# Kernel tuning notes

Hardware: AMD Instinct MI355X
Metric: run time of the kernel (lower is better)

## Reference

```python
import jax, jax.numpy as jnp
import numpy as np


def _2div(arr):
    arr_res = arr.copy()
    arr_pieces = []
    pa = 0
    st = 0
    needdivcnt = 0
    for i, a in enumerate(arr):
        if a != pa:
            arr_pieces.append([st, i])
            if i - st != 1:
                needdivcnt += 1
            pa = a
            st = i
    arr_pieces.append([st, len(arr)])
    if len(arr) - st != 1:
        needdivcnt += 1
    offset = range(len(arr_pieces), len(arr_pieces) + needdivcnt)
    p = 0
    for arr_p in arr_pieces:
        length = arr_p[1] - arr_p[0]
        if length == 1:
            continue
        half_len = int(np.ceil(length / 2))
        for j in range(arr_p[0] + half_len, arr_p[1]):
            arr_res[j] = offset[p]
        p += 1
    return arr_res


def get_division_tree(n_agents):
    agent2divitreeindex = np.arange(n_agents)
    np.random.shuffle(agent2divitreeindex)
    max_div = np.ceil(np.log2(n_agents)).astype(int)
    levels = np.zeros(shape=(max_div + 1, n_agents), dtype=int)
    for ith in range(1, len(levels)):
        levels[ith, :] = _2div(levels[ith - 1, :])
    res_levels = levels.copy()
    for i, idx in enumerate(agent2divitreeindex):
        res_levels[:, i] = levels[:, idx]
    return res_levels


def setup_inputs() -> dict:
    B, A, H, NACT = 2048, 50, 512, 64
    F = H + A  # in-features of first Linear (hidden + one-hot agent id)
    np.random.seed(0)
    div_tree = get_division_tree(A)
    routing = jnp.asarray(div_tree[-1], dtype=jnp.int32)  # max_level routing: agent -> net index
    key = jax.random.key(0)
    k0, k1, k2 = jax.random.split(key, 3)
    x_in = jax.random.normal(k0, (B, A, H), dtype=jnp.float32)
    # stacked per-net parameters (n_nets == n_agent independent 2-layer MLPs)
    W1 = jax.random.normal(k1, (A, F, H), dtype=jnp.float32) * (1.0 / np.sqrt(F))
    b1 = jnp.zeros((A, H), dtype=jnp.float32)
    W2 = jax.random.normal(k2, (A, H, NACT), dtype=jnp.float32) * (1.0 / np.sqrt(H))
    b2 = jnp.zeros((A, NACT), dtype=jnp.float32)
    return {"x_in": x_in, "W1": W1, "b1": b1, "W2": W2, "b2": b2, "routing": routing}


def reference(x_in, W1, b1, W2, b2, routing):
    # x_in: [B, A, H]; routing: [A] int (which net each agent uses)
    B, A, H = x_in.shape
    # add_onehot_id_at_last_dim: append agent-id one-hot -> [B, A, H+A]
    onehot = jnp.broadcast_to(jnp.eye(A, dtype=x_in.dtype), (B, A, A))
    x0 = jnp.concatenate([x_in, onehot], axis=-1)
    # gather routed expert weights per agent
    W1r, b1r = W1[routing], b1[routing]   # [A, H+A, H], [A, H]
    W2r, b2r = W2[routing], b2[routing]   # [A, H, NACT], [A, NACT]
    h = jax.nn.relu(jnp.einsum('baf,afh->bah', x0, W1r) + b1r)
    out = jnp.einsum('bah,ahn->ban', h, W2r) + b2r  # [B, A, NACT]
    return out
```

## Files before the change

kernel.cpp:

```cpp
#include <hip/hip_runtime.h>

typedef __attribute__((ext_vector_type(8))) short bf16x8;
typedef __attribute__((ext_vector_type(4))) float f32x4;
typedef __attribute__((ext_vector_type(4))) unsigned short u16x4;
typedef __attribute__((ext_vector_type(8))) unsigned short u16x8;

#define B_ 2048
#define A_ 50
#define H_ 512
#define NACT_ 64
#define F_ 562
#define BM_ 64
#define BK_ 32
#define NSTEP_ (H_ / BK_)

#define WS_W1T 0
#define WS_W2T ((size_t)A_ * H_ * H_ * 2)
#define WS_B1 (WS_W2T + (size_t)A_ * NACT_ * H_ * 2)
#define WS_B2 (WS_B1 + (size_t)A_ * H_ * 4)

static __device__ __forceinline__ unsigned short f2bf(float f) {
  unsigned int u = __builtin_bit_cast(unsigned int, f);
  u += 0x7fffu + ((u >> 16) & 1u);
  return (unsigned short)(u >> 16);
}

static __device__ __forceinline__ void gld_lds16(const unsigned short* src,
                                                 unsigned short* dst) {
  __builtin_amdgcn_global_load_lds(
      (const __attribute__((address_space(1))) unsigned int*)(const void*)src,
      (__attribute__((address_space(3))) unsigned int*)(void*)dst, 16, 0, 0);
}

static __device__ __forceinline__ int clamp_r(int r) {
  return r < 0 ? 0 : (r > A_ - 1 ? A_ - 1 : r);
}

__global__ void prep_w1(const float* __restrict__ w1,
                        const int* __restrict__ routing,
                        unsigned short* __restrict__ w1t) {
  const int bid = blockIdx.x;
  const int a = bid / 64;
  const int tile = bid - a * 64;
  const int tk = tile & 7, tj = tile >> 3;
  const int k0 = tk * 64, j0 = tj * 64;
  const int r = clamp_r(routing[a]);
  __shared__ float tl[64][65];
  const int t = threadIdx.x;
  const int c = t & 63, q = t >> 6;
#pragma unroll
  for (int i = 0; i < 16; ++i) {
    const int kl = q + i * 4;
    tl[kl][c] = w1[((size_t)r * F_ + k0 + kl) * H_ + j0 + c];
  }
  __syncthreads();
#pragma unroll
  for (int it = 0; it < 2; ++it) {
    const int jl = t >> 2, c2 = t & 3;
    const int kc = it * 4 + (c2 ^ (jl & 3));
    u16x8 v;
#pragma unroll
    for (int e = 0; e < 8; ++e) v[e] = f2bf(tl[kc * 8 + e][jl]);
    unsigned short* dst = w1t +
        (((size_t)a * 16 + tk * 2 + it) * H_ + j0 + jl) * 32 + c2 * 8;
    *(u16x8*)dst = v;
  }
}

__global__ void prep_w2(const float* __restrict__ w2,
                        const int* __restrict__ routing,
                        unsigned short* __restrict__ w2t) {
  const int bid = blockIdx.x;
  const int a = bid >> 3;
  const int tk = bid & 7;
  const int k0 = tk * 64;
  const int r = clamp_r(routing[a]);
  __shared__ float tl[64][65];
  const int t = threadIdx.x;
  const int c = t & 63, q = t >> 6;
#pragma unroll
  for (int i = 0; i < 16; ++i) {
    const int kl = q + i * 4;
    tl[kl][c] = w2[((size_t)r * H_ + k0 + kl) * NACT_ + c];
  }
  __syncthreads();
#pragma unroll
  for (int i = 0; i < 16; ++i) {
    const int nl = q + i * 4;
    w2t[((size_t)a * NACT_ + nl) * H_ + k0 + c] = f2bf(tl[c][nl]);
  }
}

__global__ void prep_bias(const float* __restrict__ w1,
                          const float* __restrict__ b1,
                          const float* __restrict__ b2,
                          const int* __restrict__ routing,
                          float* __restrict__ bias1, float* __restrict__ bias2) {
  const int a = blockIdx.x;
  const int t = threadIdx.x;
  const int r = clamp_r(routing[a]);
  bias1[a * H_ + t] = b1[(size_t)r * H_ + t] + w1[((size_t)r * F_ + H_ + a) * H_ + t];
  if (t < NACT_) bias2[a * NACT_ + t] = b2[r * NACT_ + t];
}

__global__ __launch_bounds__(512, 4) void divtree_main(
    const float* __restrict__ x, const unsigned short* __restrict__ w1t,
    const unsigned short* __restrict__ w2t, const float* __restrict__ bias1,
    const float* __restrict__ bias2, float* __restrict__ out) {
  __shared__ union {
    struct {
      unsigned short w1[2][H_ * BK_];
      unsigned short xs[2][BM_ * BK_];
    } st;
    unsigned short h[BM_ * H_];
    float outb[BM_][66];
  } sm;

  const int bid = blockIdx.x;
  const int swz = (bid & 7) * 200 + (bid >> 3);
  const int a = swz >> 5;
  const int mblk = swz & 31;
  const int b0 = mblk * BM_;

  const int tid = threadIdx.x;
  const int lane = tid & 63;
  const int w = tid >> 6;
  const int l16 = lane & 15;
  const int lk = lane >> 4;
  const int sxor = lk ^ (l16 & 3);

  const int wj = w * 64;

  const unsigned short* w1ta = w1t + (size_t)a * (H_ * H_);

  const int xrow = tid >> 3;
  const int xq = tid & 7;
  const float* xbase =
      x + ((size_t)(b0 + xrow) * A_ + (size_t)a) * H_ + (size_t)xq * 4;
  const int xs_off = xrow * BK_ + ((xq >> 1) ^ (xrow & 3)) * 8 + (xq & 1) * 4;

  const int afr_base = (wj + l16) * BK_ + sxor * 8;
  const int bfr_base = l16 * BK_ + sxor * 8;

  f32x4 acc[4][4];
#pragma unroll
  for (int i = 0; i < 4; ++i)
#pragma unroll
    for (int j = 0; j < 4; ++j) acc[i][j] = (f32x4){0.f, 0.f, 0.f, 0.f};

  f32x4 xr[3];

  {
    const f32x4 xv0 = *(const f32x4*)xbase;
#pragma unroll
    for (int i = 0; i < 4; ++i)
      gld_lds16(w1ta + ((size_t)(i * 512 + tid) << 3),
                sm.st.w1[0] + (size_t)(i * 512 + (w << 6)) * 8);
    xr[1] = *(const f32x4*)(xbase + 1 * BK_);
    xr[2] = *(const f32x4*)(xbase + 2 * BK_);
    u16x4 v;
#pragma unroll
    for (int e = 0; e < 4; ++e) v[e] = f2bf(xv0[e]);
    *(u16x4*)(sm.st.xs[0] + xs_off) = v;
  }

#pragma unroll
  for (int t = 0; t < NSTEP_; ++t) {
    const int buf = t & 1;
    if (t <= NSTEP_ - 3)
      asm volatile("s_waitcnt vmcnt(1) lgkmcnt(0)" ::: "memory");
    else
      asm volatile("s_waitcnt vmcnt(0) lgkmcnt(0)" ::: "memory");
    __builtin_amdgcn_sched_barrier(0);
    __builtin_amdgcn_s_barrier();
    __builtin_amdgcn_sched_barrier(0);
    if (t + 1 < NSTEP_) {
      const unsigned short* wsrc = w1ta + (size_t)(t + 1) * (H_ * BK_);
      unsigned short* wdst = sm.st.w1[buf ^ 1];
#pragma unroll
      for (int i = 0; i < 4; ++i)
        gld_lds16(wsrc + ((size_t)(i * 512 + tid) << 3),
                  wdst + (size_t)(i * 512 + (w << 6)) * 8);
    }
    if (t + 3 < NSTEP_)
      xr[(t + 3) % 3] = *(const f32x4*)(xbase + (size_t)(t + 3) * BK_);
    const unsigned short* w1s = sm.st.w1[buf];
    const unsigned short* xss = sm.st.xs[buf];
    bf16x8 bfr[4];
#pragma unroll
    for (int mf = 0; mf < 4; ++mf)
      bfr[mf] = *(const bf16x8*)(xss + bfr_base + mf * (16 * BK_));
    __builtin_amdgcn_s_setprio(1);
#pragma unroll
    for (int jf = 0; jf < 4; ++jf) {
      const bf16x8 afr = *(const bf16x8*)(w1s + afr_base + jf * (16 * BK_));
#pragma unroll
      for (int mf = 0; mf < 4; ++mf)
        acc[jf][mf] = __builtin_amdgcn_mfma_f32_16x16x32_bf16(
            afr, bfr[mf], acc[jf][mf], 0, 0, 0);
    }
    __builtin_amdgcn_s_setprio(0);
    if (t + 1 < NSTEP_) {
      const f32x4 xv = xr[(t + 1) % 3];
      u16x4 v;
#pragma unroll
      for (int e = 0; e < 4; ++e) v[e] = f2bf(xv[e]);
      *(u16x4*)(sm.st.xs[buf ^ 1] + xs_off) = v;
    }
  }
  __syncthreads();

  const float* b1p = bias1 + a * H_;
#pragma unroll
  for (int jf = 0; jf < 4; ++jf) {
    const f32x4 bv = *(const f32x4*)(b1p + wj + jf * 16 + lk * 4);
    const int cbase = (wj >> 3) + jf * 2 + (lk >> 1);
    const int half4 = (lk & 1) * 4;
#pragma unroll
    for (int mf = 0; mf < 4; ++mf) {
      u16x4 hv;
#pragma unroll
      for (int r = 0; r < 4; ++r) {
        float f = acc[jf][mf][r] + bv[r];
        f = f > 0.f ? f : 0.f;
        hv[r] = f2bf(f);
      }
      const int m = mf * 16 + l16;
      const int off = m * H_ + ((cbase ^ (l16 & 7))) * 8 + half4;
      *(u16x4*)(sm.h + off) = hv;
    }
  }
  __syncthreads();

  const int m0 = (w & 1) * 32;
  const int n0 = (w >> 1) * 16;
  const unsigned short* w2p =
      w2t + ((size_t)a * NACT_ + n0 + l16) * H_ + lk * 8;
  f32x4 acc2[2];
  acc2[0] = (f32x4){0.f, 0.f, 0.f, 0.f};
  acc2[1] = (f32x4){0.f, 0.f, 0.f, 0.f};
#pragma unroll
  for (int kf = 0; kf < 16; ++kf) {
    const bf16x8 bf2 = *(const bf16x8*)(w2p + kf * 32);
#pragma unroll
    for (int mf = 0; mf < 2; ++mf) {
      const int row = m0 + mf * 16 + l16;
      const int off = row * H_ + (((kf * 4 + lk) ^ (l16 & 7))) * 8;
      const bf16x8 af2 = *(const bf16x8*)(sm.h + off);
      acc2[mf] = __builtin_amdgcn_mfma_f32_16x16x32_bf16(af2, bf2, acc2[mf],
                                                         0, 0, 0);
    }
  }
  const float b2v = bias2[a * NACT_ + n0 + l16];
  __syncthreads();
#pragma unroll
  for (int mf = 0; mf < 2; ++mf)
#pragma unroll
    for (int r = 0; r < 4; ++r)
      sm.outb[m0 + mf * 16 + lk * 4 + r][n0 + l16] = acc2[mf][r] + b2v;
  __syncthreads();

  {
    const int row = tid >> 3;
    const int q8 = (tid & 7) * 8;
    const f32x4 v0 = *(const f32x4*)(&sm.outb[row][q8]);
    const f32x4 v1 = *(const f32x4*)(&sm.outb[row][q8 + 4]);
    float* op = out + ((size_t)(b0 + row) * A_ + a) * NACT_ + q8;
    *(f32x4*)op = v0;
    *(f32x4*)(op + 4) = v1;
  }
}

extern "C" void kernel_launch(void* const* d_in, const int* in_sizes, int n_in,
                              void* d_out, int out_size, void* d_ws,
                              size_t ws_size, hipStream_t stream) {
  const float* x = (const float*)d_in[0];
  const float* w1 = (const float*)d_in[1];
  const float* b1 = (const float*)d_in[2];
  const float* w2 = (const float*)d_in[3];
  const float* b2 = (const float*)d_in[4];
  const int* routing = (const int*)d_in[5];
  float* out = (float*)d_out;

  char* ws = (char*)d_ws;
  unsigned short* w1t = (unsigned short*)(ws + WS_W1T);
  unsigned short* w2t = (unsigned short*)(ws + WS_W2T);
  float* bias1 = (float*)(ws + WS_B1);
  float* bias2 = (float*)(ws + WS_B2);

  prep_w1<<<A_ * 64, 256, 0, stream>>>(w1, routing, w1t);
  prep_w2<<<A_ * 8, 256, 0, stream>>>(w2, routing, w2t);
  prep_bias<<<A_, 512, 0, stream>>>(w1, b1, b2, routing, bias1, bias2);
  divtree_main<<<A_ * (B_ / BM_), 512, 0, stream>>>(x, w1t, w2t, bias1, bias2,
                                                    out);
}
```

Baseline: 143.2 us.

## Double tile to BM=128, BK=64 with single-buffered x and split-K barriers

Doubles the batch rows per block to 128 and the K-step to 64, so each block reuses every streamed W1 tile across twice as many rows and does half as many pipeline steps. The W1 workspace layout and its XOR swizzle change to match the 64-wide K chunk. The x tile goes from double-buffered to single-buffered, with a mid-step barrier placed so the next x tile can be written after the second half-K of reads, and the second-layer GEMM is retiled across 8 waves. Accumulator registers per thread double and occupancy drops to 2 blocks per CU (launch bound 4 to 2), and there are half as many blocks, which may hurt latency hiding and leave the GPU less evenly loaded.

```diff
diff --git a/kernel.cpp b/kernel.cpp
--- a/kernel.cpp
+++ b/kernel.cpp
@@ -10,8 +10,8 @@
 #define H_ 512
 #define NACT_ 64
 #define F_ 562
-#define BM_ 64
-#define BK_ 32
+#define BM_ 128
+#define BK_ 64
 #define NSTEP_ (H_ / BK_)
 
 #define WS_W1T 0
@@ -57,12 +57,13 @@
 #pragma unroll
   for (int it = 0; it < 2; ++it) {
     const int jl = t >> 2, c2 = t & 3;
-    const int kc = it * 4 + (c2 ^ (jl & 3));
+    const int p = it * 4 + c2;
+    const int cl = p ^ (jl & 7);
     u16x8 v;
 #pragma unroll
-    for (int e = 0; e < 8; ++e) v[e] = f2bf(tl[kc * 8 + e][jl]);
-    unsigned short* dst = w1t +
-        (((size_t)a * 16 + tk * 2 + it) * H_ + j0 + jl) * 32 + c2 * 8;
+    for (int e = 0; e < 8; ++e) v[e] = f2bf(tl[cl * 8 + e][jl]);
+    unsigned short* dst =
+        w1t + (((size_t)a * 8 + tk) * H_ + j0 + jl) * 64 + p * 8;
     *(u16x8*)dst = v;
   }
 }
@@ -103,23 +104,23 @@
   if (t < NACT_) bias2[a * NACT_ + t] = b2[r * NACT_ + t];
 }
 
-__global__ __launch_bounds__(512, 4) void divtree_main(
+__global__ __launch_bounds__(512, 2) void divtree_main(
     const float* __restrict__ x, const unsigned short* __restrict__ w1t,
     const unsigned short* __restrict__ w2t, const float* __restrict__ bias1,
     const float* __restrict__ bias2, float* __restrict__ out) {
   __shared__ union {
     struct {
       unsigned short w1[2][H_ * BK_];
-      unsigned short xs[2][BM_ * BK_];
+      unsigned short xs[BM_ * BK_];
     } st;
     unsigned short h[BM_ * H_];
     float outb[BM_][66];
   } sm;
 
   const int bid = blockIdx.x;
-  const int swz = (bid & 7) * 200 + (bid >> 3);
-  const int a = swz >> 5;
-  const int mblk = swz & 31;
+  const int swz = (bid & 7) * 100 + (bid >> 3);
+  const int a = swz >> 4;
+  const int mblk = swz & 15;
   const int b0 = mblk * BM_;
 
   const int tid = threadIdx.x;
@@ -127,94 +128,140 @@
   const int w = tid >> 6;
   const int l16 = lane & 15;
   const int lk = lane >> 4;
-  const int sxor = lk ^ (l16 & 3);
-
-  const int wj = w * 64;
+  const int l7 = l16 & 7;
+
+  const int wnq = w & 3;
+  const int wm = w >> 2;
 
   const unsigned short* w1ta = w1t + (size_t)a * (H_ * H_);
 
-  const int xrow = tid >> 3;
-  const int xq = tid & 7;
+  const int xrow = tid >> 2;
+  const int xseg = tid & 3;
   const float* xbase =
-      x + ((size_t)(b0 + xrow) * A_ + (size_t)a) * H_ + (size_t)xq * 4;
-  const int xs_off = xrow * BK_ + ((xq >> 1) ^ (xrow & 3)) * 8 + (xq & 1) * 4;
-
-  const int afr_base = (wj + l16) * BK_ + sxor * 8;
-  const int bfr_base = l16 * BK_ + sxor * 8;
-
-  f32x4 acc[4][4];
-#pragma unroll
-  for (int i = 0; i < 4; ++i)
+      x + ((size_t)(b0 + xrow) * A_ + (size_t)a) * H_ + (size_t)xseg * 16;
+  const int xp0 = (xseg * 2) ^ (xrow & 7);
+  const int xp1 = (xseg * 2 + 1) ^ (xrow & 7);
+  unsigned short* xs0 = sm.st.xs + xrow * BK_;
+
+  f32x4 acc[8][4];
+#pragma unroll
+  for (int i = 0; i < 8; ++i)
 #pragma unroll
     for (int j = 0; j < 4; ++j) acc[i][j] = (f32x4){0.f, 0.f, 0.f, 0.f};
 
-  f32x4 xr[3];
+  f32x4 xr[2][4];
 
   {
-    const f32x4 xv0 = *(const f32x4*)xbase;
-#pragma unroll
-    for (int i = 0; i < 4; ++i)
+    f32x4 x0[4];
+#pragma unroll
+    for (int i = 0; i < 4; ++i) x0[i] = *(const f32x4*)(xbase + i * 4);
+#pragma unroll
+    for (int i = 0; i < 8; ++i)
       gld_lds16(w1ta + ((size_t)(i * 512 + tid) << 3),
                 sm.st.w1[0] + (size_t)(i * 512 + (w << 6)) * 8);
-    xr[1] = *(const f32x4*)(xbase + 1 * BK_);
-    xr[2] = *(const f32x4*)(xbase + 2 * BK_);
-    u16x4 v;
-#pragma unroll
-    for (int e = 0; e < 4; ++e) v[e] = f2bf(xv0[e]);
-    *(u16x4*)(sm.st.xs[0] + xs_off) = v;
+    u16x8 v0, v1;
+#pragma unroll
+    for (int e = 0; e < 4; ++e) {
+      v0[e] = f2bf(x0[0][e]); v0[4 + e] = f2bf(x0[1][e]);
+      v1[e] = f2bf(x0[2][e]); v1[4 + e] = f2bf(x0[3][e]);
+    }
+    *(u16x8*)(xs0 + xp0 * 8) = v0;
+    *(u16x8*)(xs0 + xp1 * 8) = v1;
+#pragma unroll
+    for (int i = 0; i < 4; ++i)
+      xr[1][i] = *(const f32x4*)(xbase + 1 * BK_ + i * 4);
+    asm volatile("s_waitcnt vmcnt(4) lgkmcnt(0)" ::: "memory");
+    __builtin_amdgcn_sched_barrier(0);
+    __builtin_amdgcn_s_barrier();
+    __builtin_amdgcn_sched_barrier(0);
   }
 
 #pragma unroll
   for (int t = 0; t < NSTEP_; ++t) {
     const int buf = t & 1;
-    if (t <= NSTEP_ - 3)
-      asm volatile("s_waitcnt vmcnt(1) lgkmcnt(0)" ::: "memory");
+    if (t + 1 < NSTEP_) {
+      const unsigned short* wsrc = w1ta + (size_t)(t + 1) * (H_ * BK_);
+      unsigned short* wdst = sm.st.w1[buf ^ 1];
+#pragma unroll
+      for (int i = 0; i < 8; ++i)
+        gld_lds16(wsrc + ((size_t)(i * 512 + tid) << 3),
+                  wdst + (size_t)(i * 512 + (w << 6)) * 8);
+    }
+    const unsigned short* w1s = sm.st.w1[buf];
+    {
+      bf16x8 afr[8], bfr[4];
+#pragma unroll
+      for (int jf = 0; jf < 8; ++jf)
+        afr[jf] = *(const bf16x8*)(w1s + (wnq * 128 + jf * 16 + l16) * 64 +
+                                   ((0 * 4 + lk) ^ l7) * 8);
+#pragma unroll
+      for (int mf = 0; mf < 4; ++mf)
+        bfr[mf] = *(const bf16x8*)(sm.st.xs + (wm * 64 + mf * 16 + l16) * 64 +
+                                   ((0 * 4 + lk) ^ l7) * 8);
+      __builtin_amdgcn_s_setprio(1);
+#pragma unroll
+      for (int jf = 0; jf < 8; ++jf)
+#pragma unroll
+        for (int mf = 0; mf < 4; ++mf)
+          acc[jf][mf] = __builtin_amdgcn_mfma_f32_16x16x32_bf16(
+              afr[jf], bfr[mf], acc[jf][mf], 0, 0, 0);
+      __builtin_amdgcn_s_setprio(0);
+    }
+    {
+      bf16x8 afr[8], bfr[4];
+#pragma unroll
+      for (int jf = 0; jf < 8; ++jf)
+        afr[jf] = *(const bf16x8*)(w1s + (wnq * 128 + jf * 16 + l16) * 64 +
+                                   ((1 * 4 + lk) ^ l7) * 8);
+#pragma unroll
+      for (int mf = 0; mf < 4; ++mf)
+        bfr[mf] = *(const bf16x8*)(sm.st.xs + (wm * 64 + mf * 16 + l16) * 64 +
+                                   ((1 * 4 + lk) ^ l7) * 8);
+      asm volatile("s_waitcnt lgkmcnt(0)" ::: "memory");
+      __builtin_amdgcn_sched_barrier(0);
+      __builtin_amdgcn_s_barrier();
+      __builtin_amdgcn_s_setprio(1);
+#pragma unroll
+      for (int jf = 0; jf < 8; ++jf)
+#pragma unroll
+        for (int mf = 0; mf < 4; ++mf)
+          acc[jf][mf] = __builtin_amdgcn_mfma_f32_16x16x32_bf16(
+              afr[jf], bfr[mf], acc[jf][mf], 0, 0, 0);
+      __builtin_amdgcn_s_setprio(0);
+    }
+    if (t + 1 < NSTEP_) {
+      asm volatile("s_waitcnt vmcnt(8)" ::: "memory");
+      __builtin_amdgcn_sched_barrier(0);
+      u16x8 v0, v1;
+#pragma unroll
+      for (int e = 0; e < 4; ++e) {
+        v0[e] = f2bf(xr[(t + 1) & 1][0][e]);
+        v0[4 + e] = f2bf(xr[(t + 1) & 1][1][e]);
+        v1[e] = f2bf(xr[(t + 1) & 1][2][e]);
+        v1[4 + e] = f2bf(xr[(t + 1) & 1][3][e]);
+      }
+      *(u16x8*)(xs0 + xp0 * 8) = v0;
+      *(u16x8*)(xs0 + xp1 * 8) = v1;
+    }
+    if (t + 2 < NSTEP_) {
+#pragma unroll
+      for (int i = 0; i < 4; ++i)
+        xr[t & 1][i] = *(const f32x4*)(xbase + (size_t)(t + 2) * BK_ + i * 4);
+    }
+    if (t + 2 < NSTEP_)
+      asm volatile("s_waitcnt vmcnt(4) lgkmcnt(0)" ::: "memory");
     else
       asm volatile("s_waitcnt vmcnt(0) lgkmcnt(0)" ::: "memory");
     __builtin_amdgcn_sched_barrier(0);
     __builtin_amdgcn_s_barrier();
     __builtin_amdgcn_sched_barrier(0);
-    if (t + 1 < NSTEP_) {
-      const unsigned short* wsrc = w1ta + (size_t)(t + 1) * (H_ * BK_);
-      unsigned short* wdst = sm.st.w1[buf ^ 1];
-#pragma unroll
-      for (int i = 0; i < 4; ++i)
-        gld_lds16(wsrc + ((size_t)(i * 512 + tid) << 3),
-                  wdst + (size_t)(i * 512 + (w << 6)) * 8);
-    }
-    if (t + 3 < NSTEP_)
-      xr[(t + 3) % 3] = *(const f32x4*)(xbase + (size_t)(t + 3) * BK_);
-    const unsigned short* w1s = sm.st.w1[buf];
-    const unsigned short* xss = sm.st.xs[buf];
-    bf16x8 bfr[4];
-#pragma unroll
-    for (int mf = 0; mf < 4; ++mf)
-      bfr[mf] = *(const bf16x8*)(xss + bfr_base + mf * (16 * BK_));
-    __builtin_amdgcn_s_setprio(1);
-#pragma unroll
-    for (int jf = 0; jf < 4; ++jf) {
-      const bf16x8 afr = *(const bf16x8*)(w1s + afr_base + jf * (16 * BK_));
-#pragma unroll
-      for (int mf = 0; mf < 4; ++mf)
-        acc[jf][mf] = __builtin_amdgcn_mfma_f32_16x16x32_bf16(
-            afr, bfr[mf], acc[jf][mf], 0, 0, 0);
-    }
-    __builtin_amdgcn_s_setprio(0);
-    if (t + 1 < NSTEP_) {
-      const f32x4 xv = xr[(t + 1) % 3];
-      u16x4 v;
-#pragma unroll
-      for (int e = 0; e < 4; ++e) v[e] = f2bf(xv[e]);
-      *(u16x4*)(sm.st.xs[buf ^ 1] + xs_off) = v;
-    }
-  }
-  __syncthreads();
+  }
 
   const float* b1p = bias1 + a * H_;
 #pragma unroll
-  for (int jf = 0; jf < 4; ++jf) {
-    const f32x4 bv = *(const f32x4*)(b1p + wj + jf * 16 + lk * 4);
-    const int cbase = (wj >> 3) + jf * 2 + (lk >> 1);
+  for (int jf = 0; jf < 8; ++jf) {
+    const f32x4 bv = *(const f32x4*)(b1p + wnq * 128 + jf * 16 + lk * 4);
+    const int cJ = wnq * 16 + jf * 2 + (lk >> 1);
     const int half4 = (lk & 1) * 4;
 #pragma unroll
     for (int mf = 0; mf < 4; ++mf) {
@@ -225,49 +272,63 @@
         f = f > 0.f ? f : 0.f;
         hv[r] = f2bf(f);
       }
-      const int m = mf * 16 + l16;
-      const int off = m * H_ + ((cbase ^ (l16 & 7))) * 8 + half4;
+      const int m = wm * 64 + mf * 16 + l16;
+      const int off = m * H_ + ((cJ ^ (m & 7))) * 8 + half4;
       *(u16x4*)(sm.h + off) = hv;
     }
   }
   __syncthreads();
 
-  const int m0 = (w & 1) * 32;
-  const int n0 = (w >> 1) * 16;
-  const unsigned short* w2p =
-      w2t + ((size_t)a * NACT_ + n0 + l16) * H_ + lk * 8;
-  f32x4 acc2[2];
-  acc2[0] = (f32x4){0.f, 0.f, 0.f, 0.f};
-  acc2[1] = (f32x4){0.f, 0.f, 0.f, 0.f};
+  const int m0 = (w >> 1) * 32;
+  const int n0 = (w & 1) * 32;
+  f32x4 acc2[2][2];
+#pragma unroll
+  for (int i = 0; i < 2; ++i)
+#pragma unroll
+    for (int j = 0; j < 2; ++j) acc2[i][j] = (f32x4){0.f, 0.f, 0.f, 0.f};
 #pragma unroll
   for (int kf = 0; kf < 16; ++kf) {
-    const bf16x8 bf2 = *(const bf16x8*)(w2p + kf * 32);
+    bf16x8 bf2[2], af2[2];
+#pragma unroll
+    for (int nf = 0; nf < 2; ++nf)
+      bf2[nf] = *(const bf16x8*)(w2t +
+                                 ((size_t)a * NACT_ + n0 + nf * 16 + l16) * H_ +
+                                 kf * 32 + lk * 8);
 #pragma unroll
     for (int mf = 0; mf < 2; ++mf) {
       const int row = m0 + mf * 16 + l16;
-      const int off = row * H_ + (((kf * 4 + lk) ^ (l16 & 7))) * 8;
-      const bf16x8 af2 = *(const bf16x8*)(sm.h + off);
-      acc2[mf] = __builtin_amdgcn_mfma_f32_16x16x32_bf16(af2, bf2, acc2[mf],
-                                                         0, 0, 0);
-    }
-  }
-  const float b2v = bias2[a * NACT_ + n0 + l16];
+      af2[mf] = *(const bf16x8*)(sm.h + row * H_ +
+                                 (((kf * 4 + lk) ^ (l16 & 7))) * 8);
+    }
+#pragma unroll
+    for (int mf = 0; mf < 2; ++mf)
+#pragma unroll
+      for (int nf = 0; nf < 2; ++nf)
+        acc2[mf][nf] = __builtin_amdgcn_mfma_f32_16x16x32_bf16(
+            af2[mf], bf2[nf], acc2[mf][nf], 0, 0, 0);
+  }
+  float b2v[2];
+#pragma unroll
+  for (int nf = 0; nf < 2; ++nf)
+    b2v[nf] = bias2[a * NACT_ + n0 + nf * 16 + l16];
   __syncthreads();
 #pragma unroll
   for (int mf = 0; mf < 2; ++mf)
 #pragma unroll
-    for (int r = 0; r < 4; ++r)
-      sm.outb[m0 + mf * 16 + lk * 4 + r][n0 + l16] = acc2[mf][r] + b2v;
+    for (int nf = 0; nf < 2; ++nf)
+#pragma unroll
+      for (int r = 0; r < 4; ++r)
+        sm.outb[m0 + mf * 16 + lk * 4 + r][n0 + nf * 16 + l16] =
+            acc2[mf][nf][r] + b2v[nf];
   __syncthreads();
 
   {
-    const int row = tid >> 3;
-    const int q8 = (tid & 7) * 8;
-    const f32x4 v0 = *(const f32x4*)(&sm.outb[row][q8]);
-    const f32x4 v1 = *(const f32x4*)(&sm.outb[row][q8 + 4]);
-    float* op = out + ((size_t)(b0 + row) * A_ + a) * NACT_ + q8;
-    *(f32x4*)op = v0;
-    *(f32x4*)(op + 4) = v1;
+    const int row = tid >> 2;
+    const int sg = (tid & 3) * 16;
+    float* op = out + ((size_t)(b0 + row) * A_ + a) * NACT_ + sg;
+#pragma unroll
+    for (int i = 0; i < 4; ++i)
+      *(f32x4*)(op + i * 4) = *(const f32x4*)(&sm.outb[row][sg + i * 4]);
   }
 }
 
```

After: 174.8 us. +22.1%, slower.

## Split fused MLP into two tiled GEMM kernels with a bf16 hidden buffer

Applied to the files above, without the earlier changes.

Replaces the single fused kernel, which handled 64 batch rows against the full 512-wide hidden layer, with two kernels. The first computes layer 1 in 128x128 tiles and writes bf16 hidden activations to workspace. The second reads them back for layer 2 in 128-row tiles with a reswizzled W2 layout. The intent is more reuse per tile and better occupancy. The cost is an extra round trip of about 100MB of hidden activations through global memory, and the new path only runs when the workspace is large enough, otherwise it falls back to the old kernel.

```diff
diff --git a/kernel.cpp b/kernel.cpp
--- a/kernel.cpp
+++ b/kernel.cpp
@@ -10,14 +10,13 @@
 #define H_ 512
 #define NACT_ 64
 #define F_ 562
-#define BM_ 64
-#define BK_ 32
-#define NSTEP_ (H_ / BK_)
 
 #define WS_W1T 0
 #define WS_W2T ((size_t)A_ * H_ * H_ * 2)
 #define WS_B1 (WS_W2T + (size_t)A_ * NACT_ * H_ * 2)
 #define WS_B2 (WS_B1 + (size_t)A_ * H_ * 4)
+#define WS_H (WS_B2 + (size_t)A_ * NACT_ * 4)
+#define WS_NEED (WS_H + (size_t)B_ * A_ * H_ * 2)
 
 static __device__ __forceinline__ unsigned short f2bf(float f) {
   unsigned int u = __builtin_bit_cast(unsigned int, f);
@@ -36,9 +35,9 @@
   return r < 0 ? 0 : (r > A_ - 1 ? A_ - 1 : r);
 }
 
-__global__ void prep_w1(const float* __restrict__ w1,
-                        const int* __restrict__ routing,
-                        unsigned short* __restrict__ w1t) {
+__global__ void prep_w1_n(const float* __restrict__ w1,
+                          const int* __restrict__ routing,
+                          unsigned short* __restrict__ w1t) {
   const int bid = blockIdx.x;
   const int a = bid / 64;
   const int tile = bid - a * 64;
@@ -54,22 +53,23 @@
     tl[kl][c] = w1[((size_t)r * F_ + k0 + kl) * H_ + j0 + c];
   }
   __syncthreads();
+  const int jl = t >> 2, pq = t & 3;
+  const int sx = (jl >> 1) & 3;
 #pragma unroll
   for (int it = 0; it < 2; ++it) {
-    const int jl = t >> 2, c2 = t & 3;
-    const int kc = it * 4 + (c2 ^ (jl & 3));
+    const int cc = pq ^ sx;
     u16x8 v;
 #pragma unroll
-    for (int e = 0; e < 8; ++e) v[e] = f2bf(tl[kc * 8 + e][jl]);
-    unsigned short* dst = w1t +
-        (((size_t)a * 16 + tk * 2 + it) * H_ + j0 + jl) * 32 + c2 * 8;
+    for (int e = 0; e < 8; ++e) v[e] = f2bf(tl[it * 32 + cc * 8 + e][jl]);
+    unsigned short* dst =
+        w1t + (((size_t)a * 16 + tk * 2 + it) * H_ + j0 + jl) * 32 + pq * 8;
     *(u16x8*)dst = v;
   }
 }
 
-__global__ void prep_w2(const float* __restrict__ w2,
-                        const int* __restrict__ routing,
-                        unsigned short* __restrict__ w2t) {
+__global__ void prep_w2_n(const float* __restrict__ w2,
+                          const int* __restrict__ routing,
+                          unsigned short* __restrict__ w2t) {
   const int bid = blockIdx.x;
   const int a = bid >> 3;
   const int tk = bid & 7;
@@ -84,10 +84,17 @@
     tl[kl][c] = w2[((size_t)r * H_ + k0 + kl) * NACT_ + c];
   }
   __syncthreads();
-#pragma unroll
-  for (int i = 0; i < 16; ++i) {
-    const int nl = q + i * 4;
-    w2t[((size_t)a * NACT_ + nl) * H_ + k0 + c] = f2bf(tl[c][nl]);
+  const int n = t >> 2, pq0 = t & 3;
+#pragma unroll
+  for (int it = 0; it < 2; ++it) {
+    const int p = it * 4 + pq0;
+    const int cc = p ^ (n & 7);
+    u16x8 v;
+#pragma unroll
+    for (int e = 0; e < 8; ++e) v[e] = f2bf(tl[cc * 8 + e][n]);
+    unsigned short* dst =
+        w2t + (((size_t)a * 8 + tk) * NACT_ + n) * 64 + p * 8;
+    *(u16x8*)dst = v;
   }
 }
 
@@ -103,104 +110,410 @@
   if (t < NACT_) bias2[a * NACT_ + t] = b2[r * NACT_ + t];
 }
 
-__global__ __launch_bounds__(512, 4) void divtree_main(
+__global__ __launch_bounds__(256, 3) void k1_l1(
+    const float* __restrict__ x, const unsigned short* __restrict__ w1t,
+    const float* __restrict__ bias1, unsigned short* __restrict__ h_ws) {
+  __shared__ union {
+    struct {
+      unsigned short w1s[2][128 * 32];
+      unsigned short xs[2][128 * 32];
+    } st;
+    unsigned short hl[128 * 128];
+  } sm;
+
+  const int bid = blockIdx.x;
+  const int swz = (bid & 7) * 400 + (bid >> 3);
+  const int a = swz >> 6;
+  const int rem = swz & 63;
+  const int mt = rem >> 2, jt = rem & 3;
+  const int b0 = mt * 128, j0g = jt * 128;
+
+  const int tid = threadIdx.x;
+  const int lane = tid & 63;
+  const int w = tid >> 6;
+  const int l16 = lane & 15;
+  const int lk = lane >> 4;
+  const int sxor = lk ^ ((l16 >> 1) & 3);
+
+  const int wj = (w & 1) * 64, wm = (w >> 1) * 64;
+
+  const unsigned short* w1src =
+      w1t + (size_t)a * (16 * H_ * 32) + (size_t)j0g * 32;
+
+  const int xrow = tid >> 1, xhalf = tid & 1;
+  const float* xp =
+      x + ((size_t)(b0 + xrow) * A_ + (size_t)a) * H_ + xhalf * 16;
+  const int xsrow = xrow * 32;
+  const int xpos0 = (xhalf * 2) ^ ((xrow >> 1) & 3);
+
+  const int afr_off = (wj + l16) * 32 + sxor * 8;
+  const int bfr_off = (wm + l16) * 32 + sxor * 8;
+
+  f32x4 acc[4][4];
+#pragma unroll
+  for (int i = 0; i < 4; ++i)
+#pragma unroll
+    for (int j = 0; j < 4; ++j) acc[i][j] = (f32x4){0.f, 0.f, 0.f, 0.f};
+
+  {
+    f32x4 xv[4];
+#pragma unroll
+    for (int i = 0; i < 4; ++i) xv[i] = *(const f32x4*)(xp + i * 4);
+#pragma unroll
+    for (int i = 0; i < 2; ++i) {
+      const int idx = i * 256 + tid;
+      gld_lds16(w1src + (size_t)(idx >> 2) * 32 + (idx & 3) * 8,
+                sm.st.w1s[0] + idx * 8);
+    }
+    u16x8 v0, v1;
+#pragma unroll
+    for (int e = 0; e < 4; ++e) {
+      v0[e] = f2bf(xv[0][e]); v0[4 + e] = f2bf(xv[1][e]);
+      v1[e] = f2bf(xv[2][e]); v1[4 + e] = f2bf(xv[3][e]);
+    }
+    *(u16x8*)(sm.st.xs[0] + xsrow + xpos0 * 8) = v0;
+    *(u16x8*)(sm.st.xs[0] + xsrow + (xpos0 ^ 1) * 8) = v1;
+  }
+  __syncthreads();
+
+#pragma unroll 2
+  for (int t = 0; t < 16; ++t) {
+    const int buf = t & 1;
+    f32x4 xv[4];
+    if (t < 15) {
+      const float* p = xp + (t + 1) * 32;
+#pragma unroll
+      for (int i = 0; i < 4; ++i) xv[i] = *(const f32x4*)(p + i * 4);
+      const unsigned short* wsrc = w1src + (size_t)(t + 1) * (H_ * 32);
+#pragma unroll
+      for (int i = 0; i < 2; ++i) {
+        const int idx = i * 256 + tid;
+        gld_lds16(wsrc + (size_t)(idx >> 2) * 32 + (idx & 3) * 8,
+                  sm.st.w1s[buf ^ 1] + idx * 8);
+      }
+    }
+    {
+      const unsigned short* w1s = sm.st.w1s[buf];
+      const unsigned short* xss = sm.st.xs[buf];
+      bf16x8 afr[4], bfr[4];
+#pragma unroll
+      for (int jf = 0; jf < 4; ++jf)
+        afr[jf] = *(const bf16x8*)(w1s + afr_off + jf * (16 * 32));
+#pragma unroll
+      for (int mf = 0; mf < 4; ++mf)
+        bfr[mf] = *(const bf16x8*)(xss + bfr_off + mf * (16 * 32));
+#pragma unroll
+      for (int jf = 0; jf < 4; ++jf)
+#pragma unroll
+        for (int mf = 0; mf < 4; ++mf)
+          acc[jf][mf] = __builtin_amdgcn_mfma_f32_16x16x32_bf16(
+              afr[jf], bfr[mf], acc[jf][mf], 0, 0, 0);
+    }
+    if (t < 15) {
+      u16x8 v0, v1;
+#pragma unroll
+      for (int e = 0; e < 4; ++e) {
+        v0[e] = f2bf(xv[0][e]); v0[4 + e] = f2bf(xv[1][e]);
+        v1[e] = f2bf(xv[2][e]); v1[4 + e] = f2bf(xv[3][e]);
+      }
+      *(u16x8*)(sm.st.xs[buf ^ 1] + xsrow + xpos0 * 8) = v0;
+      *(u16x8*)(sm.st.xs[buf ^ 1] + xsrow + (xpos0 ^ 1) * 8) = v1;
+    }
+    __syncthreads();
+  }
+
+  const float* b1p = bias1 + a * H_ + j0g;
+#pragma unroll
+  for (int jf = 0; jf < 4; ++jf) {
+    const f32x4 bv = *(const f32x4*)(b1p + wj + jf * 16 + lk * 4);
+    const int cJ = (wj >> 3) + jf * 2 + (lk >> 1);
+    const int half4 = (lk & 1) * 4;
+#pragma unroll
+    for (int mf = 0; mf < 4; ++mf) {
+      u16x4 hv;
+#pragma unroll
+      for (int r = 0; r < 4; ++r) {
+        float f = acc[jf][mf][r] + bv[r];
+        f = f > 0.f ? f : 0.f;
+        hv[r] = f2bf(f);
+      }
+      const int m = wm + mf * 16 + l16;
+      const int p = (cJ & 8) | ((cJ & 7) ^ (m & 7));
+      *(u16x4*)(sm.hl + m * 128 + p * 8 + half4) = hv;
+    }
+  }
+  __syncthreads();
+  {
+    const int m = tid >> 1, half = tid & 1;
+    unsigned short* rowbase =
+        h_ws + ((size_t)a * B_ + b0 + m) * H_ + (jt * 2 + half) * 64;
+    const unsigned short* lsrc = sm.hl + m * 128 + half * 64;
+#pragma unroll
+    for (int p = 0; p < 8; ++p)
+      *(u16x8*)(rowbase + p * 8) = *(const u16x8*)(lsrc + p * 8);
+  }
+}
+
+__global__ __launch_bounds__(256, 3) void k2_l2(
+    const unsigned short* __restrict__ h_ws,
+    const unsigned short* __restrict__ w2t, const float* __restrict__ bias2,
+    float* __restrict__ out) {
+  __shared__ union {
+    struct {
+      unsigned short hA[2][128 * 64];
+      unsigned short wB[2][64 * 64];
+    } st;
+    float outb[128][66];
+  } sm;
+
+  const int bid = blockIdx.x;
+  const int swz = (bid & 7) * 100 + (bid >> 3);
+  const int a = swz >> 4;
+  const int bt = swz & 15;
+  const int b0 = bt * 128;
+
+  const int tid = threadIdx.x;
+  const int lane = tid & 63;
+  const int w = tid >> 6;
+  const int l16 = lane & 15;
+  const int lk = lane >> 4;
+  const int wm2 = w * 32;
+
+  const unsigned short* hsrc = h_ws + ((size_t)a * B_ + b0) * H_;
+  const unsigned short* wsrc = w2t + (size_t)a * 8 * (NACT_ * 64);
+
+  f32x4 acc2[2][4];
+#pragma unroll
+  for (int i = 0; i < 2; ++i)
+#pragma unroll
+    for (int j = 0; j < 4; ++j) acc2[i][j] = (f32x4){0.f, 0.f, 0.f, 0.f};
+
+  {
+#pragma unroll
+    for (int i = 0; i < 4; ++i) {
+      const int idx = i * 256 + tid;
+      gld_lds16(hsrc + (size_t)(idx >> 3) * H_ + (idx & 7) * 8,
+                sm.st.hA[0] + idx * 8);
+    }
+#pragma unroll
+    for (int i = 0; i < 2; ++i) {
+      const int idx = i * 256 + tid;
+      gld_lds16(wsrc + (size_t)(idx >> 3) * 64 + (idx & 7) * 8,
+                sm.st.wB[0] + idx * 8);
+    }
+  }
+  __syncthreads();
+
+#pragma unroll 2
+  for (int s = 0; s < 8; ++s) {
+    const int buf = s & 1;
+    if (s < 7) {
+      const unsigned short* hs = hsrc + (s + 1) * 64;
+      const unsigned short* ws = wsrc + (size_t)(s + 1) * (NACT_ * 64);
+#pragma unroll
+      for (int i = 0; i < 4; ++i) {
+        const int idx = i * 256 + tid;
+        gld_lds16(hs + (size_t)(idx >> 3) * H_ + (idx & 7) * 8,
+                  sm.st.hA[buf ^ 1] + idx * 8);
+      }
+#pragma unroll
+      for (int i = 0; i < 2; ++i) {
+        const int idx = i * 256 + tid;
+        gld_lds16(ws + (size_t)(idx >> 3) * 64 + (idx & 7) * 8,
+                  sm.st.wB[buf ^ 1] + idx * 8);
+      }
+    }
+    const unsigned short* hA = sm.st.hA[buf];
+    const unsigned short* wB = sm.st.wB[buf];
+#pragma unroll
+    for (int kk = 0; kk < 2; ++kk) {
+      const int cxor = (kk * 4 + lk);
+      bf16x8 afr[2], bfr[4];
+#pragma unroll
+      for (int mf = 0; mf < 2; ++mf) {
+        const int row = wm2 + mf * 16 + l16;
+        afr[mf] = *(const bf16x8*)(hA + row * 64 + (cxor ^ (l16 & 7)) * 8);
+      }
+#pragma unroll
+      for (int nf = 0; nf < 4; ++nf) {
+        const int n = nf * 16 + l16;
+        bfr[nf] = *(const bf16x8*)(wB + n * 64 + (cxor ^ (l16 & 7)) * 8);
+      }
+#pragma unroll
+      for (int mf = 0; mf < 2; ++mf)
+#pragma unroll
+        for (int nf = 0; nf < 4; ++nf)
+          acc2[mf][nf] = __builtin_amdgcn_mfma_f32_16x16x32_bf16(
+              afr[mf], bfr[nf], acc2[mf][nf], 0, 0, 0);
+    }
+    __syncthreads();
+  }
+
+  float b2v[4];
+#pragma unroll
+  for (int nf = 0; nf < 4; ++nf)
+    b2v[nf] = bias2[a * NACT_ + nf * 16 + l16];
+#pragma unroll
+  for (int mf = 0; mf < 2; ++mf)
+#pragma unroll
+    for (int nf = 0; nf < 4; ++nf)
+#pragma unroll
+      for (int r = 0; r < 4; ++r)
+        sm.outb[wm2 + mf * 16 + lk * 4 + r][nf * 16 + l16] =
+            acc2[mf][nf][r] + b2v[nf];
+  __syncthreads();
+  {
+    const int row = tid >> 1, half = tid & 1;
+    float* op = out + ((size_t)(b0 + row) * A_ + a) * NACT_ + half * 32;
+#pragma unroll
+    for (int i = 0; i < 8; ++i)
+      *(f32x4*)(op + i * 4) = *(const f32x4*)(&sm.outb[row][half * 32 + i * 4]);
+  }
+}
+
+__global__ void prep_w1_fb(const float* __restrict__ w1,
+                           const int* __restrict__ routing,
+                           unsigned short* __restrict__ w1t) {
+  const int bid = blockIdx.x;
+  const int a = bid / 64;
+  const int tile = bid - a * 64;
+  const int tk = tile & 7, tj = tile >> 3;
+  const int k0 = tk * 64, j0 = tj * 64;
+  const int r = clamp_r(routing[a]);
+  __shared__ float tl[64][65];
+  const int t = threadIdx.x;
+  const int c = t & 63, q = t >> 6;
+#pragma unroll
+  for (int i = 0; i < 16; ++i) {
+    const int kl = q + i * 4;
+    tl[kl][c] = w1[((size_t)r * F_ + k0 + kl) * H_ + j0 + c];
+  }
+  __syncthreads();
+#pragma unroll
+  for (int it = 0; it < 2; ++it) {
+    const int jl = t >> 2, c2 = t & 3;
+    const int kc = it * 4 + (c2 ^ (jl & 3));
+    u16x8 v;
+#pragma unroll
+    for (int e = 0; e < 8; ++e) v[e] = f2bf(tl[kc * 8 + e][jl]);
+    unsigned short* dst = w1t +
+        (((size_t)a * 16 + tk * 2 + it) * H_ + j0 + jl) * 32 + c2 * 8;
+    *(u16x8*)dst = v;
+  }
+}
+
+__global__ void prep_w2_fb(const float* __restrict__ w2,
+                           const int* __restrict__ routing,
+                           unsigned short* __restrict__ w2t) {
+  const int bid = blockIdx.x;
+  const int a = bid >> 3;
+  const int tk = bid & 7;
+  const int k0 = tk * 64;
+  const int r = clamp_r(routing[a]);
+  __shared__ float tl[64][65];
+  const int t = threadIdx.x;
+  const int c = t & 63, q = t >> 6;
+#pragma unroll
+  for (int i = 0; i < 16; ++i) {
+    const int kl = q + i * 4;
+    tl[kl][c] = w2[((size_t)r * H_ + k0 + kl) * NACT_ + c];
+  }
+  __syncthreads();
+#pragma unroll
+  for (int i = 0; i < 16; ++i) {
+    const int nl = q + i * 4;
+    w2t[((size_t)a * NACT_ + nl) * H_ + k0 + c] = f2bf(tl[c][nl]);
+  }
+}
+
+__global__ __launch_bounds__(512, 4) void divtree_main_fb(
     const float* __restrict__ x, const unsigned short* __restrict__ w1t,
     const unsigned short* __restrict__ w2t, const float* __restrict__ bias1,
     const float* __restrict__ bias2, float* __restrict__ out) {
   __shared__ union {
     struct {
-      unsigned short w1[2][H_ * BK_];
-      unsigned short xs[2][BM_ * BK_];
+      unsigned short w1[2][H_ * 32];
+      unsigned short xs[2][64 * 32];
     } st;
-    unsigned short h[BM_ * H_];
-    float outb[BM_][66];
+    unsigned short h[64 * H_];
+    float outb[64][66];
   } sm;
-
   const int bid = blockIdx.x;
   const int swz = (bid & 7) * 200 + (bid >> 3);
   const int a = swz >> 5;
   const int mblk = swz & 31;
-  const int b0 = mblk * BM_;
-
+  const int b0 = mblk * 64;
   const int tid = threadIdx.x;
   const int lane = tid & 63;
   const int w = tid >> 6;
   const int l16 = lane & 15;
   const int lk = lane >> 4;
   const int sxor = lk ^ (l16 & 3);
-
   const int wj = w * 64;
-
   const unsigned short* w1ta = w1t + (size_t)a * (H_ * H_);
-
   const int xrow = tid >> 3;
   const int xq = tid & 7;
   const float* xbase =
       x + ((size_t)(b0 + xrow) * A_ + (size_t)a) * H_ + (size_t)xq * 4;
-  const int xs_off = xrow * BK_ + ((xq >> 1) ^ (xrow & 3)) * 8 + (xq & 1) * 4;
-
-  const int afr_base = (wj + l16) * BK_ + sxor * 8;
-  const int bfr_base = l16 * BK_ + sxor * 8;
-
+  const int xs_off = xrow * 32 + ((xq >> 1) ^ (xrow & 3)) * 8 + (xq & 1) * 4;
+  const int afr_base = (wj + l16) * 32 + sxor * 8;
+  const int bfr_base = l16 * 32 + sxor * 8;
   f32x4 acc[4][4];
 #pragma unroll
   for (int i = 0; i < 4; ++i)
 #pragma unroll
     for (int j = 0; j < 4; ++j) acc[i][j] = (f32x4){0.f, 0.f, 0.f, 0.f};
-
   f32x4 xr[3];
-
   {
     const f32x4 xv0 = *(const f32x4*)xbase;
 #pragma unroll
     for (int i = 0; i < 4; ++i)
       gld_lds16(w1ta + ((size_t)(i * 512 + tid) << 3),
                 sm.st.w1[0] + (size_t)(i * 512 + (w << 6)) * 8);
-    xr[1] = *(const f32x4*)(xbase + 1 * BK_);
-    xr[2] = *(const f32x4*)(xbase + 2 * BK_);
+    xr[1] = *(const f32x4*)(xbase + 32);
+    xr[2] = *(const f32x4*)(xbase + 64);
     u16x4 v;
 #pragma unroll
     for (int e = 0; e < 4; ++e) v[e] = f2bf(xv0[e]);
     *(u16x4*)(sm.st.xs[0] + xs_off) = v;
   }
-
-#pragma unroll
-  for (int t = 0; t < NSTEP_; ++t) {
+#pragma unroll
+  for (int t = 0; t < 16; ++t) {
     const int buf = t & 1;
-    if (t <= NSTEP_ - 3)
+    if (t <= 13)
       asm volatile("s_waitcnt vmcnt(1) lgkmcnt(0)" ::: "memory");
     else
       asm volatile("s_waitcnt vmcnt(0) lgkmcnt(0)" ::: "memory");
     __builtin_amdgcn_sched_barrier(0);
     __builtin_amdgcn_s_barrier();
     __builtin_amdgcn_sched_barrier(0);
-    if (t + 1 < NSTEP_) {
-      const unsigned short* wsrc = w1ta + (size_t)(t + 1) * (H_ * BK_);
+    if (t + 1 < 16) {
+      const unsigned short* wsrc = w1ta + (size_t)(t + 1) * (H_ * 32);
       unsigned short* wdst = sm.st.w1[buf ^ 1];
 #pragma unroll
       for (int i = 0; i < 4; ++i)
         gld_lds16(wsrc + ((size_t)(i * 512 + tid) << 3),
                   wdst + (size_t)(i * 512 + (w << 6)) * 8);
     }
-    if (t + 3 < NSTEP_)
-      xr[(t + 3) % 3] = *(const f32x4*)(xbase + (size_t)(t + 3) * BK_);
+    if (t + 3 < 16)
+      xr[(t + 3) % 3] = *(const f32x4*)(xbase + (size_t)(t + 3) * 32);
     const unsigned short* w1s = sm.st.w1[buf];
     const unsigned short* xss = sm.st.xs[buf];
     bf16x8 bfr[4];
 #pragma unroll
     for (int mf = 0; mf < 4; ++mf)
-      bfr[mf] = *(const bf16x8*)(xss + bfr_base + mf * (16 * BK_));
+      bfr[mf] = *(const bf16x8*)(xss + bfr_base + mf * (16 * 32));
     __builtin_amdgcn_s_setprio(1);
 #pragma unroll
     for (int jf = 0; jf < 4; ++jf) {
-      const bf16x8 afr = *(const bf16x8*)(w1s + afr_base + jf * (16 * BK_));
+      const bf16x8 afr = *(const bf16x8*)(w1s + afr_base + jf * (16 * 32));
 #pragma unroll
       for (int mf = 0; mf < 4; ++mf)
         acc[jf][mf] = __builtin_amdgcn_mfma_f32_16x16x32_bf16(
             afr, bfr[mf], acc[jf][mf], 0, 0, 0);
     }
     __builtin_amdgcn_s_setprio(0);
-    if (t + 1 < NSTEP_) {
+    if (t + 1 < 16) {
       const f32x4 xv = xr[(t + 1) % 3];
       u16x4 v;
 #pragma unroll
@@ -209,7 +522,6 @@
     }
   }
   __syncthreads();
-
   const float* b1p = bias1 + a * H_;
 #pragma unroll
   for (int jf = 0; jf < 4; ++jf) {
@@ -231,7 +543,6 @@
     }
   }
   __syncthreads();
-
   const int m0 = (w & 1) * 32;
   const int n0 = (w >> 1) * 16;
   const unsigned short* w2p =
@@ -259,7 +570,6 @@
     for (int r = 0; r < 4; ++r)
       sm.outb[m0 + mf * 16 + lk * 4 + r][n0 + l16] = acc2[mf][r] + b2v;
   __syncthreads();
-
   {
     const int row = tid >> 3;
     const int q8 = (tid & 7) * 8;
@@ -288,9 +598,18 @@
   float* bias1 = (float*)(ws + WS_B1);
   float* bias2 = (float*)(ws + WS_B2);
 
-  prep_w1<<<A_ * 64, 256, 0, stream>>>(w1, routing, w1t);
-  prep_w2<<<A_ * 8, 256, 0, stream>>>(w2, routing, w2t);
-  prep_bias<<<A_, 512, 0, stream>>>(w1, b1, b2, routing, bias1, bias2);
-  divtree_main<<<A_ * (B_ / BM_), 512, 0, stream>>>(x, w1t, w2t, bias1, bias2,
-                                                    out);
-}
+  if (ws_size >= WS_NEED) {
+    unsigned short* h_ws = (unsigned short*)(ws + WS_H);
+    prep_w1_n<<<A_ * 64, 256, 0, stream>>>(w1, routing, w1t);
+    prep_w2_n<<<A_ * 8, 256, 0, stream>>>(w2, routing, w2t);
+    prep_bias<<<A_, 512, 0, stream>>>(w1, b1, b2, routing, bias1, bias2);
+    k1_l1<<<A_ * 64, 256, 0, stream>>>(x, w1t, bias1, h_ws);
+    k2_l2<<<A_ * 16, 256, 0, stream>>>(h_ws, w2t, bias2, out);
+  } else {
+    prep_w1_fb<<<A_ * 64, 256, 0, stream>>>(w1, routing, w1t);
+    prep_w2_fb<<<A_ * 8, 256, 0, stream>>>(w2, routing, w2t);
+    prep_bias<<<A_, 512, 0, stream>>>(w1, b1, b2, routing, bias1, bias2);
+    divtree_main_fb<<<A_ * 32, 512, 0, stream>>>(x, w1t, w2t, bias1, bias2,
+                                                 out);
+  }
+}
```

Result: slower. 204.2 us (+42.7%).

## Preload whole X tile into LDS and triple-buffer W1 stages

Applied to the files above, without the earlier changes.

The main kernel now loads the block's entire 64x512 activation tile up front, converts it to bf16 once into a swizzled LDS buffer, and streams W1 slices through a three-deep LDS ring with two stages in flight. This removes the per-step x loads and bf16 conversions and cuts the barriers to one per step. The W1 prep kernel changes its XOR swizzle pattern to match the new LDS read addressing. The price is much more LDS per block (about 160KB), so launch bounds drop to 2 blocks per CU and occupancy may fall.

```diff
diff --git a/kernel.cpp b/kernel.cpp
--- a/kernel.cpp
+++ b/kernel.cpp
@@ -10,9 +10,6 @@
 #define H_ 512
 #define NACT_ 64
 #define F_ 562
-#define BM_ 64
-#define BK_ 32
-#define NSTEP_ (H_ / BK_)
 
 #define WS_W1T 0
 #define WS_W2T ((size_t)A_ * H_ * H_ * 2)
@@ -36,9 +33,9 @@
   return r < 0 ? 0 : (r > A_ - 1 ? A_ - 1 : r);
 }
 
-__global__ void prep_w1(const float* __restrict__ w1,
-                        const int* __restrict__ routing,
-                        unsigned short* __restrict__ w1t) {
+__global__ void prep_w1_n(const float* __restrict__ w1,
+                          const int* __restrict__ routing,
+                          unsigned short* __restrict__ w1t) {
   const int bid = blockIdx.x;
   const int a = bid / 64;
   const int tile = bid - a * 64;
@@ -54,15 +51,16 @@
     tl[kl][c] = w1[((size_t)r * F_ + k0 + kl) * H_ + j0 + c];
   }
   __syncthreads();
+  const int jl = t >> 2, pq = t & 3;
+  const int sx = (jl >> 1) & 3;
 #pragma unroll
   for (int it = 0; it < 2; ++it) {
-    const int jl = t >> 2, c2 = t & 3;
-    const int kc = it * 4 + (c2 ^ (jl & 3));
+    const int cc = pq ^ sx;
     u16x8 v;
 #pragma unroll
-    for (int e = 0; e < 8; ++e) v[e] = f2bf(tl[kc * 8 + e][jl]);
-    unsigned short* dst = w1t +
-        (((size_t)a * 16 + tk * 2 + it) * H_ + j0 + jl) * 32 + c2 * 8;
+    for (int e = 0; e < 8; ++e) v[e] = f2bf(tl[it * 32 + cc * 8 + e][jl]);
+    unsigned short* dst =
+        w1t + (((size_t)a * 16 + tk * 2 + it) * H_ + j0 + jl) * 32 + pq * 8;
     *(u16x8*)dst = v;
   }
 }
@@ -103,44 +101,44 @@
   if (t < NACT_) bias2[a * NACT_ + t] = b2[r * NACT_ + t];
 }
 
-__global__ __launch_bounds__(512, 4) void divtree_main(
+__global__ __launch_bounds__(512, 2) void divtree_v7(
     const float* __restrict__ x, const unsigned short* __restrict__ w1t,
     const unsigned short* __restrict__ w2t, const float* __restrict__ bias1,
     const float* __restrict__ bias2, float* __restrict__ out) {
   __shared__ union {
     struct {
-      unsigned short w1[2][H_ * BK_];
-      unsigned short xs[2][BM_ * BK_];
+      unsigned short xs[64 * 512];
+      unsigned short w1[3][512 * 32];
     } st;
-    unsigned short h[BM_ * H_];
-    float outb[BM_][66];
+    unsigned short h[64 * 512];
+    struct {
+      unsigned short pad[64 * 512];
+      float outb[64][66];
+    } ep;
   } sm;
 
   const int bid = blockIdx.x;
   const int swz = (bid & 7) * 200 + (bid >> 3);
   const int a = swz >> 5;
   const int mblk = swz & 31;
-  const int b0 = mblk * BM_;
+  const int b0 = mblk * 64;
 
   const int tid = threadIdx.x;
   const int lane = tid & 63;
   const int w = tid >> 6;
   const int l16 = lane & 15;
   const int lk = lane >> 4;
-  const int sxor = lk ^ (l16 & 3);
-
+  const int l7 = l16 & 7;
   const int wj = w * 64;
 
-  const unsigned short* w1ta = w1t + (size_t)a * (H_ * H_);
-
-  const int xrow = tid >> 3;
+  const unsigned short* w1ta = w1t + (size_t)a * (16 * H_ * 32);
+
+  const int xm = tid >> 3;
   const int xq = tid & 7;
-  const float* xbase =
-      x + ((size_t)(b0 + xrow) * A_ + (size_t)a) * H_ + (size_t)xq * 4;
-  const int xs_off = xrow * BK_ + ((xq >> 1) ^ (xrow & 3)) * 8 + (xq & 1) * 4;
-
-  const int afr_base = (wj + l16) * BK_ + sxor * 8;
-  const int bfr_base = l16 * BK_ + sxor * 8;
+  const float* xrowp =
+      x + ((size_t)(b0 + xm) * A_ + (size_t)a) * H_ + (size_t)xq * 64;
+
+  const int afr_base = (wj + l16) * 32 + (lk ^ ((l16 >> 1) & 3)) * 8;
 
   f32x4 acc[4][4];
 #pragma unroll
@@ -148,67 +146,71 @@
 #pragma unroll
     for (int j = 0; j < 4; ++j) acc[i][j] = (f32x4){0.f, 0.f, 0.f, 0.f};
 
-  f32x4 xr[3];
-
   {
-    const f32x4 xv0 = *(const f32x4*)xbase;
+    f32x4 xv[16];
+#pragma unroll
+    for (int i = 0; i < 16; ++i) xv[i] = *(const f32x4*)(xrowp + i * 4);
 #pragma unroll
     for (int i = 0; i < 4; ++i)
-      gld_lds16(w1ta + ((size_t)(i * 512 + tid) << 3),
-                sm.st.w1[0] + (size_t)(i * 512 + (w << 6)) * 8);
-    xr[1] = *(const f32x4*)(xbase + 1 * BK_);
-    xr[2] = *(const f32x4*)(xbase + 2 * BK_);
-    u16x4 v;
-#pragma unroll
-    for (int e = 0; e < 4; ++e) v[e] = f2bf(xv0[e]);
-    *(u16x4*)(sm.st.xs[0] + xs_off) = v;
-  }
-
-#pragma unroll
-  for (int t = 0; t < NSTEP_; ++t) {
-    const int buf = t & 1;
-    if (t <= NSTEP_ - 3)
-      asm volatile("s_waitcnt vmcnt(1) lgkmcnt(0)" ::: "memory");
-    else
-      asm volatile("s_waitcnt vmcnt(0) lgkmcnt(0)" ::: "memory");
+      gld_lds16(w1ta + (size_t)(i * 512 + tid) * 8,
+                sm.st.w1[0] + (i * 512 + tid) * 8);
+#pragma unroll
+    for (int i = 0; i < 4; ++i)
+      gld_lds16(w1ta + 16384 + (size_t)(i * 512 + tid) * 8,
+                sm.st.w1[1] + (i * 512 + tid) * 8);
+#pragma unroll
+    for (int j = 0; j < 8; ++j) {
+      u16x8 v;
+#pragma unroll
+      for (int e = 0; e < 4; ++e) {
+        v[e] = f2bf(xv[2 * j][e]);
+        v[4 + e] = f2bf(xv[2 * j + 1][e]);
+      }
+      const int c = xq * 8 + j;
+      *(u16x8*)(sm.st.xs + xm * 512 + (c ^ (xm & 7)) * 8) = v;
+    }
+    asm volatile("s_waitcnt vmcnt(4) lgkmcnt(0)" ::: "memory");
     __builtin_amdgcn_sched_barrier(0);
     __builtin_amdgcn_s_barrier();
     __builtin_amdgcn_sched_barrier(0);
-    if (t + 1 < NSTEP_) {
-      const unsigned short* wsrc = w1ta + (size_t)(t + 1) * (H_ * BK_);
-      unsigned short* wdst = sm.st.w1[buf ^ 1];
+  }
+
+#pragma unroll
+  for (int t = 0; t < 16; ++t) {
+    const int buf = t % 3;
+    if (t + 2 < 16) {
+      const unsigned short* src = w1ta + (size_t)(t + 2) * 16384;
+      unsigned short* dst = sm.st.w1[(t + 2) % 3];
 #pragma unroll
       for (int i = 0; i < 4; ++i)
-        gld_lds16(wsrc + ((size_t)(i * 512 + tid) << 3),
-                  wdst + (size_t)(i * 512 + (w << 6)) * 8);
-    }
-    if (t + 3 < NSTEP_)
-      xr[(t + 3) % 3] = *(const f32x4*)(xbase + (size_t)(t + 3) * BK_);
+        gld_lds16(src + (size_t)(i * 512 + tid) * 8,
+                  dst + (i * 512 + tid) * 8);
+    }
     const unsigned short* w1s = sm.st.w1[buf];
-    const unsigned short* xss = sm.st.xs[buf];
-    bf16x8 bfr[4];
+    bf16x8 afr[4], bfr[4];
+#pragma unroll
+    for (int jf = 0; jf < 4; ++jf)
+      afr[jf] = *(const bf16x8*)(w1s + afr_base + jf * 512);
+    const int post = ((t * 4 + lk) ^ l7) * 8;
 #pragma unroll
     for (int mf = 0; mf < 4; ++mf)
-      bfr[mf] = *(const bf16x8*)(xss + bfr_base + mf * (16 * BK_));
+      bfr[mf] = *(const bf16x8*)(sm.st.xs + (mf * 16 + l16) * 512 + post);
     __builtin_amdgcn_s_setprio(1);
 #pragma unroll
-    for (int jf = 0; jf < 4; ++jf) {
-      const bf16x8 afr = *(const bf16x8*)(w1s + afr_base + jf * (16 * BK_));
+    for (int jf = 0; jf < 4; ++jf)
 #pragma unroll
       for (int mf = 0; mf < 4; ++mf)
         acc[jf][mf] = __builtin_amdgcn_mfma_f32_16x16x32_bf16(
-            afr, bfr[mf], acc[jf][mf], 0, 0, 0);
-    }
+            afr[jf], bfr[mf], acc[jf][mf], 0, 0, 0);
     __builtin_amdgcn_s_setprio(0);
-    if (t + 1 < NSTEP_) {
-      const f32x4 xv = xr[(t + 1) % 3];
-      u16x4 v;
-#pragma unroll
-      for (int e = 0; e < 4; ++e) v[e] = f2bf(xv[e]);
-      *(u16x4*)(sm.st.xs[buf ^ 1] + xs_off) = v;
-    }
-  }
-  __syncthreads();
+    if (t + 2 < 16)
+      asm volatile("s_waitcnt vmcnt(4)" ::: "memory");
+    else
+      asm volatile("s_waitcnt vmcnt(0)" ::: "memory");
+    __builtin_amdgcn_sched_barrier(0);
+    __builtin_amdgcn_s_barrier();
+    __builtin_amdgcn_sched_barrier(0);
+  }
 
   const float* b1p = bias1 + a * H_;
 #pragma unroll
@@ -257,14 +259,14 @@
   for (int mf = 0; mf < 2; ++mf)
 #pragma unroll
     for (int r = 0; r < 4; ++r)
-      sm.outb[m0 + mf * 16 + lk * 4 + r][n0 + l16] = acc2[mf][r] + b2v;
+      sm.ep.outb[m0 + mf * 16 + lk * 4 + r][n0 + l16] = acc2[mf][r] + b2v;
   __syncthreads();
 
   {
     const int row = tid >> 3;
     const int q8 = (tid & 7) * 8;
-    const f32x4 v0 = *(const f32x4*)(&sm.outb[row][q8]);
-    const f32x4 v1 = *(const f32x4*)(&sm.outb[row][q8 + 4]);
+    const f32x4 v0 = *(const f32x4*)(&sm.ep.outb[row][q8]);
+    const f32x4 v1 = *(const f32x4*)(&sm.ep.outb[row][q8 + 4]);
     float* op = out + ((size_t)(b0 + row) * A_ + a) * NACT_ + q8;
     *(f32x4*)op = v0;
     *(f32x4*)(op + 4) = v1;
@@ -288,9 +290,8 @@
   float* bias1 = (float*)(ws + WS_B1);
   float* bias2 = (float*)(ws + WS_B2);
 
-  prep_w1<<<A_ * 64, 256, 0, stream>>>(w1, routing, w1t);
+  prep_w1_n<<<A_ * 64, 256, 0, stream>>>(w1, routing, w1t);
   prep_w2<<<A_ * 8, 256, 0, stream>>>(w2, routing, w2t);
   prep_bias<<<A_, 512, 0, stream>>>(w1, b1, b2, routing, bias1, bias2);
-  divtree_main<<<A_ * (B_ / BM_), 512, 0, stream>>>(x, w1t, w2t, bias1, bias2,
-                                                    out);
-}
+  divtree_v7<<<A_ * 32, 512, 0, stream>>>(x, w1t, w2t, bias1, bias2, out);
+}
```

Result: slower. 228.0 us (+59.3%).
